# Optimization experiments

Hardware: AMD Instinct MI355X
Metric: run time of the kernel (lower is better)

The kernel has to match this reference:

```python
import jax, jax.numpy as jnp
import numpy as np

DIM = 512
MAX_LEN = 2048
SHARED = 128
EXPAND = 2 * DIM  # expansion_factor * dim
PROJ = 2 * EXPAND + SHARED
EPS = 1e-6
BATCH = 8


def _rope(x):
    # x: [n, d]; rotates last dim (split-half RoPE) with position along axis 0
    n, d = x.shape
    half = d // 2
    freq = jnp.arange(half, dtype=x.dtype) / float(half)
    inv_freq = 10000.0 ** (-freq)
    sinusoid = jnp.arange(n, dtype=x.dtype)[:, None] * inv_freq[None, :]  # [n, half]
    sin, cos = jnp.sin(sinusoid), jnp.cos(sinusoid)
    x1, x2 = x[:, :half], x[:, half:]
    return jnp.concatenate([x1 * cos - x2 * sin, x2 * cos + x1 * sin], axis=-1)


def _toeplitz_rope(n, a, b):
    # a, b: [max_len]; tile to [n, max_len], rope over positions, then outer product
    ar = _rope(jnp.tile(a[None, :], (n, 1)))
    br = _rope(jnp.tile(b[None, :], (n, 1)))
    return jnp.einsum('mk,nk->mn', ar, br)  # [n, n]


def setup_inputs() -> dict:
    key = jax.random.key(0)
    ks = jax.random.split(key, 8)
    std = 0.02
    return {
        'x': jax.random.normal(ks[0], (BATCH, MAX_LEN, DIM), jnp.float32),
        'W1': std * jax.random.normal(ks[1], (DIM, PROJ), jnp.float32),
        'b1': jnp.zeros((PROJ,), jnp.float32),
        'W2': std * jax.random.normal(ks[2], (EXPAND, DIM), jnp.float32),
        'b2': jnp.zeros((DIM,), jnp.float32),
        'rope_a': std * jax.random.normal(ks[3], (MAX_LEN,), jnp.float32),
        'rope_b': std * jax.random.normal(ks[4], (MAX_LEN,), jnp.float32),
        'gamma': std * jax.random.normal(ks[5], (2, SHARED), jnp.float32),
        'beta': jnp.zeros((2, SHARED), jnp.float32),
        'norm_scale': jnp.asarray(1.0, jnp.float32),
    }


def reference(x, W1, b1, W2, b2, rope_a, rope_b, gamma, beta, norm_scale):
    shortcut = x
    # ScaledNorm: x * rsqrt(mean(x^2)) * scale
    ms = jnp.mean(jnp.square(x), axis=-1, keepdims=True)
    xn = x * jax.lax.rsqrt(ms + EPS) * norm_scale
    # proj1 with swish activation
    uv = jax.nn.swish(xn @ W1 + b1)  # [b, n, PROJ]
    u = uv[..., :EXPAND]
    v = uv[..., EXPAND:2 * EXPAND]
    base = uv[..., 2 * EXPAND:]  # [b, n, SHARED]
    qk_base = base[:, :, None, :] * gamma + beta  # [b, n, 2, SHARED]
    q, k = qk_base[:, :, 0, :], qk_base[:, :, 1, :]
    qk = jnp.einsum('bnd,bmd->bnm', q, k) / float(MAX_LEN)
    qk = qk + _toeplitz_rope(MAX_LEN, rope_a, rope_b)
    kernel = jnp.square(jax.nn.relu(qk))  # sqrrelu
    o = u * jnp.einsum('bnm,bme->bne', kernel, v)
    return o @ W2 + b2 + shortcut
```

## Files before the change

kernel.cpp:

```cpp
#include <hip/hip_runtime.h>
#include <math.h>

#define SEQ    2048
#define DIMM   512
#define SH     128
#define EXP    1024
#define PROJ_  2176
#define NBATCH 8
#define ROWS   16384

#define KER_SCALE     16384.0f
#define KER_SCALE_INV (1.0f / 16384.0f)
#define QK_INV        (1.0f / (4096.0f * 2048.0f))
#define W8            64.0f
#define INV4096       (1.0f / 4096.0f)

typedef __attribute__((ext_vector_type(4))) float floatx4;
typedef __attribute__((ext_vector_type(8))) int   int8v;

__device__ __forceinline__ unsigned short f2bf(float f) {
  union { float f; unsigned int u; } v; v.f = f;
  unsigned int r = (v.u + 0x7fffu + ((v.u >> 16) & 1u)) >> 16;
  return (unsigned short)r;
}
__device__ __forceinline__ float bf2f(unsigned short h) {
  union { unsigned int u; float f; } v; v.u = ((unsigned int)h) << 16;
  return v.f;
}
__device__ __forceinline__ unsigned char f2fp8(float f) {
  return (unsigned char)(__builtin_amdgcn_cvt_pk_fp8_f32(f, 0.0f, 0, false) & 0xffu);
}
__device__ __forceinline__ unsigned int pk4fp8(float a, float b, float c, float d) {
  unsigned int w = __builtin_amdgcn_cvt_pk_fp8_f32(a, b, 0, false);
  return __builtin_amdgcn_cvt_pk_fp8_f32(c, d, w, true);
}
__device__ __forceinline__ float fp82f(unsigned char b) {
  int e = (b >> 3) & 15, m = b & 7;
  float v = ldexpf((float)(e ? (8 + m) : m), (e ? e : 1) - 10);
  return (b & 0x80) ? -v : v;
}

__device__ __forceinline__ void async16(const void* g, void* l) {
  __builtin_amdgcn_global_load_lds(
      (const __attribute__((address_space(1))) void*)g,
      (__attribute__((address_space(3))) void*)l, 16, 0, 0);
}

__device__ __forceinline__ void transpose_tile_fp8(const float* __restrict__ in,
                                                   unsigned char* __restrict__ out,
                                                   int R, int C, int bx, int by, float* tile) {
  int tx = threadIdx.x & 31, ty = threadIdx.x >> 5;
  int c0 = bx * 32, r0 = by * 32;
  #pragma unroll
  for (int j = 0; j < 32; j += 8)
    tile[(ty + j) * 33 + tx] = in[(long)(r0 + ty + j) * C + c0 + tx];
  __syncthreads();
  #pragma unroll
  for (int j = 0; j < 32; j += 8)
    out[(long)(c0 + ty + j) * R + r0 + tx] = f2fp8(tile[tx * 33 + ty + j] * W8);
}

__global__ void prep_kernel(const float* __restrict__ x, const float* __restrict__ ns,
                            unsigned char* __restrict__ xq,
                            const float* __restrict__ W1, unsigned char* __restrict__ w1q,
                            const float* __restrict__ W2, unsigned char* __restrict__ w2q,
                            const float* __restrict__ ra, const float* __restrict__ rb,
                            float* __restrict__ tpl) {
  __shared__ float sh[33 * 32];
  const int b = blockIdx.x, tid = threadIdx.x;
  if (b < 4096) {
    int wave = tid >> 6, lane = tid & 63;
    long row = (long)b * 4 + wave;
    const float4* xr = (const float4*)(x + row * DIMM);
    float4 v0 = xr[lane], v1 = xr[lane + 64];
    float ss = v0.x*v0.x + v0.y*v0.y + v0.z*v0.z + v0.w*v0.w
             + v1.x*v1.x + v1.y*v1.y + v1.z*v1.z + v1.w*v1.w;
    #pragma unroll
    for (int o = 32; o > 0; o >>= 1) ss += __shfl_xor(ss, o);
    float sc = rsqrtf(ss * (1.0f / DIMM) + 1e-6f) * ns[0] * W8;
    uint2 pk;
    pk.x = pk4fp8(v0.x*sc, v0.y*sc, v0.z*sc, v0.w*sc);
    pk.y = pk4fp8(v1.x*sc, v1.y*sc, v1.z*sc, v1.w*sc);
    ((uint2*)(xq + row * DIMM))[lane] = pk;
  } else if (b < 6144) {
    const int d = b - 4096;
    float sc_ = 0.0f, ss_ = 0.0f;
    for (int k = tid; k < 1024; k += 256) {
      float a1 = ra[k], a2 = ra[k + 1024];
      float b1v = rb[k], b2v = rb[k + 1024];
      float p = a1 * b1v + a2 * b2v;
      float q = a1 * b2v - a2 * b1v;
      float th = exp2f((float)k * (-13.287712379549449f / 1024.0f));
      float ang = (float)d * th;
      sc_ += p * cosf(ang);
      ss_ += q * sinf(ang);
    }
    #pragma unroll
    for (int o = 32; o > 0; o >>= 1) {
      sc_ += __shfl_xor(sc_, o);
      ss_ += __shfl_xor(ss_, o);
    }
    int wave = tid >> 6, lane = tid & 63;
    if (lane == 0) { sh[wave] = sc_; sh[8 + wave] = ss_; }
    __syncthreads();
    if (tid == 0) {
      float Sc = sh[0] + sh[1] + sh[2] + sh[3];
      float Ss = sh[8] + sh[9] + sh[10] + sh[11];
      tpl[2047 + d] = Sc + Ss;
      if (d > 0) tpl[2047 - d] = Sc - Ss;
    }
  } else if (b < 7232) {
    int t = b - 6144;
    transpose_tile_fp8(W1, w1q, DIMM, PROJ_, t % 68, t / 68, sh);
  } else {
    int t = b - 7232;
    transpose_tile_fp8(W2, w2q, EXP, DIMM, t % 16, t / 16, sh);
  }
}

__device__ __forceinline__ void mfma_core_mx(const unsigned char* __restrict__ A,
                                             const unsigned char* __restrict__ B,
                                             int K, long rowBase, long colBase,
                                             unsigned char* smem, floatx4 acc[4][4]) {
  const int tid  = threadIdx.x;
  const int wave = tid >> 6;
  const int lane = tid & 63;
  const int wr   = (wave >> 1) * 64;
  const int wc   = (wave & 1) * 64;
  const int r_l  = lane >> 3;
  const int c8   = lane & 7;
  const int fm   = lane & 15;
  const int fq   = lane >> 4;

  floatx4 z = {0.0f, 0.0f, 0.0f, 0.0f};
  #pragma unroll
  for (int mi = 0; mi < 4; ++mi)
    #pragma unroll
    for (int ni = 0; ni < 4; ++ni) acc[mi][ni] = z;

  const unsigned char* aSrc[4];
  const unsigned char* bSrc[4];
  int ldsOff[4];
  #pragma unroll
  for (int j = 0; j < 4; ++j) {
    int row = j * 32 + wave * 8 + r_l;
    int g = c8 ^ (row & 7);
    aSrc[j] = A + (rowBase + row) * (long)K + g * 16;
    bSrc[j] = B + (colBase + row) * (long)K + g * 16;
    ldsOff[j] = (j * 32 + wave * 8) * 128;
  }

  union U8 { uint4 q[2]; int8v v; };
  const int nt = K >> 7;

  #pragma unroll
  for (int j = 0; j < 4; ++j) {
    async16(aSrc[j], smem + ldsOff[j]);
    async16(bSrc[j], smem + 16384 + ldsOff[j]);
  }
  __syncthreads();

  int cur = 0;
  for (int t = 0; t < nt; ++t) {
    unsigned char* As = smem + cur * 32768;
    unsigned char* Bs = As + 16384;
    if (t + 1 < nt) {
      unsigned char* An = smem + (cur ^ 1) * 32768;
      int k0 = (t + 1) << 7;
      #pragma unroll
      for (int j = 0; j < 4; ++j) {
        async16(aSrc[j] + k0, An + ldsOff[j]);
        async16(bSrc[j] + k0, An + 16384 + ldsOff[j]);
      }
    }
    int8v av[4], bv[4];
    #pragma unroll
    for (int mi = 0; mi < 4; ++mi) {
      int row = wr + mi * 16 + fm;
      int s0 = (2 * fq) ^ (row & 7);
      U8 u;
      u.q[0] = *(const uint4*)(As + row * 128 + s0 * 16);
      u.q[1] = *(const uint4*)(As + row * 128 + (s0 ^ 1) * 16);
      av[mi] = u.v;
    }
    #pragma unroll
    for (int ni = 0; ni < 4; ++ni) {
      int row = wc + ni * 16 + fm;
      int s0 = (2 * fq) ^ (row & 7);
      U8 u;
      u.q[0] = *(const uint4*)(Bs + row * 128 + s0 * 16);
      u.q[1] = *(const uint4*)(Bs + row * 128 + (s0 ^ 1) * 16);
      bv[ni] = u.v;
    }
    __builtin_amdgcn_s_setprio(1);
    #pragma unroll
    for (int mi = 0; mi < 4; ++mi)
      #pragma unroll
      for (int ni = 0; ni < 4; ++ni)
        acc[mi][ni] = __builtin_amdgcn_mfma_scale_f32_16x16x128_f8f6f4(
            av[mi], bv[ni], acc[mi][ni], 0, 0, 0, 0x7F7F7F7F, 0, 0x7F7F7F7F);
    __builtin_amdgcn_s_setprio(0);
    __syncthreads();
    cur ^= 1;
  }
}

#define EPILOGUE_VARS                                         \
  const int lane = threadIdx.x & 63, wave = threadIdx.x >> 6; \
  const int wr = (wave >> 1) * 64, wc = (wave & 1) * 64;      \
  const int fr = (lane >> 4) * 4, fc = lane & 15;

__global__ void __launch_bounds__(256)
gemm_uv(const unsigned char* __restrict__ xq,
        const unsigned char* __restrict__ w1q,
        const float* __restrict__ b1,
        const float* __restrict__ gamma,
        const float* __restrict__ beta,
        unsigned char* __restrict__ uq,
        unsigned char* __restrict__ vT,
        unsigned char* __restrict__ qq,
        unsigned char* __restrict__ kq) {
  __shared__ __align__(16) unsigned char smem8[65536];
  unsigned short* smem = (unsigned short*)smem8;
  floatx4 acc[4][4];
  long rowBase = (long)blockIdx.x * 128;
  long colBase = (long)blockIdx.y * 128;
  mfma_core_mx(xq, w1q, DIMM, rowBase, colBase, smem8, acc);
  EPILOGUE_VARS

  if (blockIdx.y < 8) {
    #pragma unroll
    for (int mi = 0; mi < 4; ++mi)
    #pragma unroll
    for (int ni = 0; ni < 4; ++ni)
    #pragma unroll
    for (int i = 0; i < 4; ++i) {
      long row = rowBase + wr + mi * 16 + fr + i;
      long col = colBase + wc + ni * 16 + fc;
      float t = acc[mi][ni][i] * INV4096 + b1[col];
      uq[row * EXP + col] = f2fp8(t / (1.0f + __expf(-t)) * W8);
    }
  } else if (blockIdx.y < 16) {
    __syncthreads();
    #pragma unroll
    for (int mi = 0; mi < 4; ++mi)
    #pragma unroll
    for (int ni = 0; ni < 4; ++ni)
    #pragma unroll
    for (int i = 0; i < 4; ++i) {
      int rl = wr + mi * 16 + fr + i;
      int cl = wc + ni * 16 + fc;
      long col = colBase + cl;
      float t = acc[mi][ni][i] * INV4096 + b1[col];
      smem[cl * 136 + rl] = f2bf(t / (1.0f + __expf(-t)));
    }
    __syncthreads();
    long b_   = rowBase >> 11;
    long nblk = rowBase & 2047;
    long e0   = colBase - EXP;
    #pragma unroll
    for (int rep = 0; rep < 8; ++rep) {
      int cl = rep * 16 + (threadIdx.x >> 4);
      int n0 = (threadIdx.x & 15) * 8;
      const unsigned short* src = smem + cl * 136 + n0;
      uint2 pk;
      pk.x = pk4fp8(bf2f(src[0]), bf2f(src[1]), bf2f(src[2]), bf2f(src[3]));
      pk.y = pk4fp8(bf2f(src[4]), bf2f(src[5]), bf2f(src[6]), bf2f(src[7]));
      *(uint2*)(vT + (b_ * EXP + e0 + cl) * (long)SEQ + nblk + n0) = pk;
    }
  } else {
    #pragma unroll
    for (int mi = 0; mi < 4; ++mi)
    #pragma unroll
    for (int ni = 0; ni < 4; ++ni)
    #pragma unroll
    for (int i = 0; i < 4; ++i) {
      long row = rowBase + wr + mi * 16 + fr + i;
      long col = colBase + wc + ni * 16 + fc;
      float t = acc[mi][ni][i] * INV4096 + b1[col];
      float s = t / (1.0f + __expf(-t));
      int dd = (int)(col - 2 * EXP);
      qq[row * SH + dd] = f2fp8((s * gamma[dd] + beta[dd]) * W8);
      kq[row * SH + dd] = f2fp8((s * gamma[SH + dd] + beta[SH + dd]) * W8);
    }
  }
}

__global__ void __launch_bounds__(256)
gemm_qk(const unsigned char* __restrict__ kq,
        const unsigned char* __restrict__ qq,
        const float* __restrict__ tpl,
        unsigned char* __restrict__ ker) {
  __shared__ __align__(16) unsigned char smem8[33792];
  float* tplS = (float*)(smem8 + 32768);
  floatx4 acc[4][4];
  int L = blockIdx.x;
  long b = L & 7;
  int w = L >> 3;
  long mBase = (long)(w & 15) * 128;
  long nBase = (long)(w >> 4) * 128;
  long D = nBase - mBase;
  if (threadIdx.x < 64)
    ((float4*)tplS)[threadIdx.x] = *(const float4*)(tpl + D + 1920 + 4 * (long)threadIdx.x);
  mfma_core_mx(kq + b * SEQ * SH, qq + b * SEQ * SH, SH, mBase, nBase, smem8, acc);
  unsigned char* kerb = ker + b * (long)SEQ * SEQ;
  EPILOGUE_VARS
  (void)fr;
  __syncthreads();
  #pragma unroll
  for (int mi = 0; mi < 4; ++mi)
  #pragma unroll
  for (int ni = 0; ni < 4; ++ni) {
    int m_loc0 = wr + mi * 16 + (lane >> 4) * 4;
    int n_loc  = wc + ni * 16 + fc;
    float v[4];
    #pragma unroll
    for (int i = 0; i < 4; ++i) {
      float val = acc[mi][ni][i] * QK_INV + tplS[n_loc - m_loc0 - i + 127];
      float r = fmaxf(val, 0.0f);
      v[i] = fminf(r * r * KER_SCALE, 440.0f);
    }
    *(unsigned int*)(smem8 + n_loc * 136 + m_loc0) = pk4fp8(v[0], v[1], v[2], v[3]);
  }
  __syncthreads();
  #pragma unroll
  for (int rep = 0; rep < 4; ++rep) {
    int n_loc = rep * 32 + (threadIdx.x >> 3);
    int m_seg = (threadIdx.x & 7) * 16;
    uint4 v16 = *(const uint4*)(smem8 + n_loc * 136 + m_seg);
    *(uint4*)(kerb + (nBase + n_loc) * (long)SEQ + mBase + m_seg) = v16;
  }
}

__global__ void __launch_bounds__(256)
gemm_pv(const unsigned char* __restrict__ ker,
        const unsigned char* __restrict__ vT,
        const unsigned char* __restrict__ uq,
        unsigned char* __restrict__ obq) {
  __shared__ __align__(16) unsigned char smem8[65536];
  floatx4 acc[4][4];
  int L = blockIdx.x;
  long b = L & 7;
  int w = L >> 3;
  long eBase = (long)(w & 7) * 128;
  long nBase = (long)(w >> 3) * 128;
  mfma_core_mx(vT + b * (long)EXP * SEQ, ker + b * (long)SEQ * SEQ, SEQ,
               eBase, nBase, smem8, acc);
  const unsigned char* ub = uq + b * (long)SEQ * EXP;
  unsigned char* obb = obq + b * (long)SEQ * EXP;
  EPILOGUE_VARS
  (void)fr;
  __syncthreads();
  #pragma unroll
  for (int mi = 0; mi < 4; ++mi)
  #pragma unroll
  for (int ni = 0; ni < 4; ++ni) {
    int e_loc0 = wr + mi * 16 + (lane >> 4) * 4;
    int n_loc  = wc + ni * 16 + fc;
    unsigned int uw = *(const unsigned int*)(ub + (nBase + n_loc) * (long)EXP + eBase + e_loc0);
    float v[4];
    #pragma unroll
    for (int i = 0; i < 4; ++i) {
      float u = fp82f((unsigned char)(uw >> (8 * i)));
      v[i] = acc[mi][ni][i] * KER_SCALE_INV * u;
    }
    *(unsigned int*)(smem8 + n_loc * 136 + e_loc0) = pk4fp8(v[0], v[1], v[2], v[3]);
  }
  __syncthreads();
  #pragma unroll
  for (int rep = 0; rep < 4; ++rep) {
    int n_loc = rep * 32 + (threadIdx.x >> 3);
    int e_seg = (threadIdx.x & 7) * 16;
    uint4 v16 = *(const uint4*)(smem8 + n_loc * 136 + e_seg);
    *(uint4*)(obb + (nBase + n_loc) * (long)EXP + eBase + e_seg) = v16;
  }
}

__global__ void __launch_bounds__(256)
gemm_out(const unsigned char* __restrict__ obq,
         const unsigned char* __restrict__ w2q,
         const float* __restrict__ b2,
         const float* __restrict__ x,
         float* __restrict__ out) {
  __shared__ __align__(16) unsigned char smem8[65536];
  floatx4 acc[4][4];
  long rowBase = (long)blockIdx.x * 128;
  long colBase = (long)blockIdx.y * 128;
  mfma_core_mx(obq, w2q, EXP, rowBase, colBase, smem8, acc);
  EPILOGUE_VARS
  #pragma unroll
  for (int mi = 0; mi < 4; ++mi)
  #pragma unroll
  for (int ni = 0; ni < 4; ++ni)
  #pragma unroll
  for (int i = 0; i < 4; ++i) {
    long row = rowBase + wr + mi * 16 + fr + i;
    long col = colBase + wc + ni * 16 + fc;
    out[row * DIMM + col] = acc[mi][ni][i] * INV4096 + b2[col] + x[row * DIMM + col];
  }
}

extern "C" void kernel_launch(void* const* d_in, const int* in_sizes, int n_in,
                              void* d_out, int out_size, void* d_ws, size_t ws_size,
                              hipStream_t stream) {
  const float* x          = (const float*)d_in[0];
  const float* W1         = (const float*)d_in[1];
  const float* b1         = (const float*)d_in[2];
  const float* W2         = (const float*)d_in[3];
  const float* b2         = (const float*)d_in[4];
  const float* rope_a     = (const float*)d_in[5];
  const float* rope_b     = (const float*)d_in[6];
  const float* gamma      = (const float*)d_in[7];
  const float* beta       = (const float*)d_in[8];
  const float* norm_scale = (const float*)d_in[9];
  float* out = (float*)d_out;

  char* ws = (char*)d_ws;
  size_t off = 0;
  auto nxt = [&](size_t bytes) -> void* {
    void* p = ws + off;
    off += (bytes + 255) & ~(size_t)255;
    return p;
  };
  unsigned char*  xq  = (unsigned char*)nxt((size_t)ROWS * DIMM);
  unsigned char*  w1q = (unsigned char*)nxt((size_t)PROJ_ * DIMM);
  unsigned char*  w2q = (unsigned char*)nxt((size_t)DIMM * EXP);
  unsigned char*  uq  = (unsigned char*)nxt((size_t)ROWS * EXP);
  unsigned char*  vT  = (unsigned char*)nxt((size_t)NBATCH * EXP * SEQ);
  unsigned char*  qq  = (unsigned char*)nxt((size_t)ROWS * SH);
  unsigned char*  kq  = (unsigned char*)nxt((size_t)ROWS * SH);
  float*          tpl = (float*)nxt((size_t)4096 * 4);
  unsigned char*  ker = (unsigned char*)nxt((size_t)NBATCH * SEQ * SEQ);
  unsigned char*  obq = (unsigned char*)nxt((size_t)ROWS * EXP);

  prep_kernel<<<7744, 256, 0, stream>>>(x, norm_scale, xq, W1, w1q, W2, w2q,
                                        rope_a, rope_b, tpl);
  gemm_uv<<<dim3(ROWS / 128, PROJ_ / 128), 256, 0, stream>>>(xq, w1q, b1, gamma, beta,
                                                             uq, vT, qq, kq);
  gemm_qk<<<2048, 256, 0, stream>>>(kq, qq, tpl, ker);
  gemm_pv<<<1024, 256, 0, stream>>>(ker, vT, uq, obq);
  gemm_out<<<dim3(ROWS / 128, DIMM / 128), 256, 0, stream>>>(obq, w2q, b2, x, out);
}
```

Measured before the change: 218.5 us.

## Retile PV GEMM to 256x256 double-buffered blocks with hardware FP8 decode

The kernel-times-V GEMM now uses 256x256 output tiles computed by 512-thread blocks instead of 128x128 tiles with 256 threads. Each step streams 128-wide K slices into a 128 KB double-buffered, XOR-swizzled LDS region using async global-to-LDS loads. The aim is to halve the global traffic per FLOP and overlap loads with the MFMA work. The epilogue decodes u with the hardware fp8-to-f32 conversion builtin when it is available, instead of the software bit-manipulation routine. In exchange, the grid shrinks to 256 blocks, about one per CU, and the large LDS footprint limits occupancy, so latency hiding depends entirely on the in-block pipeline.

New measurement: 221.9 us. About the same (+1.5%).

```diff
diff --git a/kernel.cpp b/kernel.cpp
--- a/kernel.cpp
+++ b/kernel.cpp
@@ -39,6 +39,23 @@
   float v = ldexpf((float)(e ? (8 + m) : m), (e ? e : 1) - 10);
   return (b & 0x80) ? -v : v;
 }
+
+#if defined(__has_builtin)
+#if __has_builtin(__builtin_amdgcn_cvt_f32_fp8)
+#define HAVE_HW_FP8DEC 1
+#endif
+#endif
+#ifdef HAVE_HW_FP8DEC
+#define FP8DEC0(w) __builtin_amdgcn_cvt_f32_fp8((w), 0)
+#define FP8DEC1(w) __builtin_amdgcn_cvt_f32_fp8((w), 1)
+#define FP8DEC2(w) __builtin_amdgcn_cvt_f32_fp8((w), 2)
+#define FP8DEC3(w) __builtin_amdgcn_cvt_f32_fp8((w), 3)
+#else
+#define FP8DEC0(w) fp82f((unsigned char)((w)))
+#define FP8DEC1(w) fp82f((unsigned char)((w) >> 8))
+#define FP8DEC2(w) fp82f((unsigned char)((w) >> 16))
+#define FP8DEC3(w) fp82f((unsigned char)((w) >> 24))
+#endif
 
 __device__ __forceinline__ void async16(const void* g, void* l) {
   __builtin_amdgcn_global_load_lds(
@@ -332,47 +349,119 @@
   }
 }
 
-__global__ void __launch_bounds__(256)
+__global__ void __launch_bounds__(512, 2)
 gemm_pv(const unsigned char* __restrict__ ker,
         const unsigned char* __restrict__ vT,
         const unsigned char* __restrict__ uq,
         unsigned char* __restrict__ obq) {
-  __shared__ __align__(16) unsigned char smem8[65536];
-  floatx4 acc[4][4];
+  __shared__ __align__(16) unsigned char smem8[131072];
+  const int tid  = threadIdx.x;
+  const int wave = tid >> 6;
+  const int lane = tid & 63;
+  const int wr2  = wave >> 2;
+  const int wc4  = wave & 3;
+  const int fm   = lane & 15;
+  const int fq   = lane >> 4;
+  const int fr   = fq * 4;
+  const int fc   = fm;
+
   int L = blockIdx.x;
   long b = L & 7;
   int w = L >> 3;
-  long eBase = (long)(w & 7) * 128;
-  long nBase = (long)(w >> 3) * 128;
-  mfma_core_mx(vT + b * (long)EXP * SEQ, ker + b * (long)SEQ * SEQ, SEQ,
-               eBase, nBase, smem8, acc);
+  long eBase = (long)(w & 3) * 256;
+  long nBase = (long)(w >> 2) * 256;
+  const unsigned char* A = vT + b * (long)EXP * SEQ;
+  const unsigned char* B = ker + b * (long)SEQ * SEQ;
+
+  floatx4 acc[8][4];
+  #pragma unroll
+  for (int mi = 0; mi < 8; ++mi)
+    #pragma unroll
+    for (int ni = 0; ni < 4; ++ni) {
+      floatx4 z = {0.0f, 0.0f, 0.0f, 0.0f};
+      acc[mi][ni] = z;
+    }
+
+  const unsigned char* src[8];
+  int ldsBase[8];
+  #pragma unroll
+  for (int j = 0; j < 8; ++j) {
+    int idx  = j * 512 + wave * 64 + lane;
+    int line = idx >> 3;
+    int row  = line & 255;
+    int c    = (idx & 7) ^ (row & 7);
+    src[j] = ((line < 256) ? (A + (eBase + row) * (long)SEQ)
+                           : (B + (nBase + row) * (long)SEQ)) + c * 16;
+    ldsBase[j] = j * 8192 + wave * 1024;
+  }
+
+  union U8 { uint4 q[2]; int8v v; };
+  const int nt = SEQ >> 7;
+
+  #pragma unroll
+  for (int j = 0; j < 8; ++j) async16(src[j], smem8 + ldsBase[j]);
+  __syncthreads();
+
+  int cur = 0;
+  for (int t = 0; t < nt; ++t) {
+    if (t + 1 < nt) {
+      unsigned char* nb = smem8 + (cur ^ 1) * 65536;
+      int k0 = (t + 1) << 7;
+      #pragma unroll
+      for (int j = 0; j < 8; ++j) async16(src[j] + k0, nb + ldsBase[j]);
+    }
+    const unsigned char* buf = smem8 + cur * 65536;
+    int8v bv[4];
+    #pragma unroll
+    for (int ni = 0; ni < 4; ++ni) {
+      int rt = wc4 * 64 + ni * 16 + fm;
+      int s0 = (2 * fq) ^ (rt & 7);
+      U8 u;
+      u.q[0] = *(const uint4*)(buf + 32768 + rt * 128 + s0 * 16);
+      u.q[1] = *(const uint4*)(buf + 32768 + rt * 128 + (s0 ^ 1) * 16);
+      bv[ni] = u.v;
+    }
+    __builtin_amdgcn_s_setprio(1);
+    #pragma unroll
+    for (int mi = 0; mi < 8; ++mi) {
+      int rt = wr2 * 128 + mi * 16 + fm;
+      int s0 = (2 * fq) ^ (rt & 7);
+      U8 a;
+      a.q[0] = *(const uint4*)(buf + rt * 128 + s0 * 16);
+      a.q[1] = *(const uint4*)(buf + rt * 128 + (s0 ^ 1) * 16);
+      #pragma unroll
+      for (int ni = 0; ni < 4; ++ni)
+        acc[mi][ni] = __builtin_amdgcn_mfma_scale_f32_16x16x128_f8f6f4(
+            a.v, bv[ni], acc[mi][ni], 0, 0, 0, 0x7F7F7F7F, 0, 0x7F7F7F7F);
+    }
+    __builtin_amdgcn_s_setprio(0);
+    __syncthreads();
+    cur ^= 1;
+  }
+
   const unsigned char* ub = uq + b * (long)SEQ * EXP;
   unsigned char* obb = obq + b * (long)SEQ * EXP;
-  EPILOGUE_VARS
-  (void)fr;
+  #pragma unroll
+  for (int mi = 0; mi < 8; ++mi)
+  #pragma unroll
+  for (int ni = 0; ni < 4; ++ni) {
+    int e_loc0 = wr2 * 128 + mi * 16 + fr;
+    int n_loc  = wc4 * 64 + ni * 16 + fc;
+    unsigned int uw = *(const unsigned int*)(ub + (nBase + n_loc) * (long)EXP + eBase + e_loc0);
+    float u0 = FP8DEC0(uw), u1 = FP8DEC1(uw), u2 = FP8DEC2(uw), u3 = FP8DEC3(uw);
+    float v0 = acc[mi][ni][0] * KER_SCALE_INV * u0;
+    float v1 = acc[mi][ni][1] * KER_SCALE_INV * u1;
+    float v2 = acc[mi][ni][2] * KER_SCALE_INV * u2;
+    float v3 = acc[mi][ni][3] * KER_SCALE_INV * u3;
+    *(unsigned int*)(smem8 + n_loc * 272 + e_loc0) = pk4fp8(v0, v1, v2, v3);
+  }
   __syncthreads();
   #pragma unroll
-  for (int mi = 0; mi < 4; ++mi)
-  #pragma unroll
-  for (int ni = 0; ni < 4; ++ni) {
-    int e_loc0 = wr + mi * 16 + (lane >> 4) * 4;
-    int n_loc  = wc + ni * 16 + fc;
-    unsigned int uw = *(const unsigned int*)(ub + (nBase + n_loc) * (long)EXP + eBase + e_loc0);
-    float v[4];
-    #pragma unroll
-    for (int i = 0; i < 4; ++i) {
-      float u = fp82f((unsigned char)(uw >> (8 * i)));
-      v[i] = acc[mi][ni][i] * KER_SCALE_INV * u;
-    }
-    *(unsigned int*)(smem8 + n_loc * 136 + e_loc0) = pk4fp8(v[0], v[1], v[2], v[3]);
-  }
-  __syncthreads();
-  #pragma unroll
-  for (int rep = 0; rep < 4; ++rep) {
-    int n_loc = rep * 32 + (threadIdx.x >> 3);
-    int e_seg = (threadIdx.x & 7) * 16;
-    uint4 v16 = *(const uint4*)(smem8 + n_loc * 136 + e_seg);
-    *(uint4*)(obb + (nBase + n_loc) * (long)EXP + eBase + e_seg) = v16;
+  for (int k = 0; k < 8; ++k) {
+    int n   = k * 32 + (tid >> 4);
+    int seg = (tid & 15) * 16;
+    uint4 v16 = *(const uint4*)(smem8 + n * 272 + seg);
+    *(uint4*)(obb + (nBase + n) * (long)EXP + eBase + seg) = v16;
   }
 }
 
@@ -438,6 +527,6 @@
   gemm_uv<<<dim3(ROWS / 128, PROJ_ / 128), 256, 0, stream>>>(xq, w1q, b1, gamma, beta,
                                                              uq, vT, qq, kq);
   gemm_qk<<<2048, 256, 0, stream>>>(kq, qq, tpl, ker);
-  gemm_pv<<<1024, 256, 0, stream>>>(ker, vT, uq, obq);
+  gemm_pv<<<256, 512, 0, stream>>>(ker, vT, uq, obq);
   gemm_out<<<dim3(ROWS / 128, DIMM / 128), 256, 0, stream>>>(obq, w2q, b2, x, out);
 }
```
